# Performance work log

Measured on AMD Instinct MI355X. Metric: run time of the kernel, lower is better.

The kernel has to match this reference:

```python
import jax, jax.numpy as jnp
import numpy as np

N_NODES = 100000


def gcn_conv(x, edge_index, edge_weight, W, b):
    """PyG GCNConv: add self-loops (weight 1), symmetric deg^-1/2 norm,
    linear transform, scatter-add aggregation over destination nodes, + bias."""
    n = x.shape[0]
    src = jnp.concatenate([edge_index[0], jnp.arange(n, dtype=edge_index.dtype)])
    dst = jnp.concatenate([edge_index[1], jnp.arange(n, dtype=edge_index.dtype)])
    ew = jnp.concatenate([edge_weight, jnp.ones((n,), dtype=x.dtype)])
    # weighted degree over destinations (symmetric graph assumed as in GCN norm)
    deg = jax.ops.segment_sum(ew, dst, num_segments=n)
    dinv = jnp.where(deg > 0, jax.lax.rsqrt(deg), 0.0).astype(x.dtype)
    norm = dinv[src] * ew * dinv[dst]                    # [E+N]
    h = x @ W                                            # [N, out]
    msg = h[src] * norm[:, None]                         # gather + scale
    agg = jax.ops.segment_sum(msg, dst, num_segments=n)  # scatter-add
    return agg + b


def setup_inputs() -> dict:
    key = jax.random.key(0)
    k = jax.random.split(key, 8)
    d_in, d_hid, d_out = 128, 64, 2
    n_edges = 3200000
    x = jax.random.normal(k[0], (N_NODES, d_in), dtype=jnp.float32)
    edge_index = jax.random.randint(k[1], (2, n_edges), 0, N_NODES, dtype=jnp.int64)
    edge_weight = jax.random.uniform(k[2], (n_edges,), dtype=jnp.float32)
    # Glorot-ish init for linear weights, zeros for bias (PyG default)
    W1 = jax.random.normal(k[3], (d_in, d_hid), dtype=jnp.float32) / np.sqrt(d_in)
    b1 = jnp.zeros((d_hid,), dtype=jnp.float32)
    W2 = jax.random.normal(k[4], (d_hid, d_out), dtype=jnp.float32) / np.sqrt(d_hid)
    b2 = jnp.zeros((d_out,), dtype=jnp.float32)
    return {"x": x, "edge_index": edge_index, "edge_weight": edge_weight,
            "W1": W1, "b1": b1, "W2": W2, "b2": b2}


def reference(x, edge_index, edge_weight, W1, b1, W2, b2):
    h = gcn_conv(x, edge_index, edge_weight, W1, b1)
    h = jax.nn.relu(h)
    out = gcn_conv(h, edge_index, edge_weight, W2, b2)
    return out
```

## Files before the change

kernel.cpp:

```cpp
#include <hip/hip_runtime.h>
#include <hip/hip_bf16.h>
#include <hip/hip_fp16.h>


#define DIN  128
#define DHID 64
#define BSH  7
#define BCAP 5000
#define SCHUNK 12544
#define BMAX 800

typedef _Float16 half8 __attribute__((ext_vector_type(8)));
typedef float    f32x4 __attribute__((ext_vector_type(4)));

__global__ __launch_bounds__(1024) void k_hist(const int* __restrict__ ei,
                                               int* __restrict__ histT,
                                               int E, int chunk, int B, int C) {
    extern __shared__ int h[];
    for (int t = threadIdx.x; t < B; t += 1024) h[t] = 0;
    __syncthreads();
    int c = blockIdx.x;
    int e0 = c * chunk, e1 = min(E, e0 + chunk);
    for (int e = e0 + threadIdx.x; e < e1; e += 1024)
        atomicAdd(&h[ei[E + e] >> BSH], 1);
    __syncthreads();
    for (int t = threadIdx.x; t < B; t += 1024) histT[(size_t)t * C + c] = h[t];
}

__global__ __launch_bounds__(256) void k_scan1(int* __restrict__ histT,
                                               int* __restrict__ tot, int C) {
    __shared__ int sm[256];
    int b = blockIdx.x, t = threadIdx.x;
    size_t base = (size_t)b * C;
    int v = histT[base + t];
    sm[t] = v;
    __syncthreads();
    for (int off = 1; off < 256; off <<= 1) {
        int add = (t >= off) ? sm[t - off] : 0;
        __syncthreads();
        sm[t] += add;
        __syncthreads();
    }
    histT[base + t] = sm[t] - v;
    if (t == 255) tot[b] = sm[t];
}

__global__ __launch_bounds__(1024) void k_scan2(const int* __restrict__ tot,
                                                int* __restrict__ bb, int B) {
    __shared__ int sm[1024];
    int t = threadIdx.x;
    int v = (t < B) ? tot[t] : 0;
    sm[t] = v;
    __syncthreads();
    for (int off = 1; off < 1024; off <<= 1) {
        int add = (t >= off) ? sm[t - off] : 0;
        __syncthreads();
        sm[t] += add;
        __syncthreads();
    }
    if (t < B) {
        bb[t] = sm[t] - v;
        if (t == B - 1) bb[B] = sm[t];
    }
}

__global__ __launch_bounds__(1024) void k_scatter(const int* __restrict__ ei,
                                                  const float* __restrict__ ew,
                                                  const int* __restrict__ histT,
                                                  const int* __restrict__ bb,
                                                  int2* __restrict__ ebuf,
                                                  int E, int chunk, int B, int C) {
    __shared__ int eidx[SCHUNK];
    __shared__ int lbase[BMAX];
    __shared__ int lcur[BMAX];
    __shared__ int gbase[BMAX];
    int c = blockIdx.x, t = threadIdx.x;
    int e0 = c * chunk, e1 = min(E, e0 + chunk), m = e1 - e0;

    for (int b = t; b < B; b += 1024) lcur[b] = 0;
    __syncthreads();
    for (int q = t; q < m; q += 1024)
        atomicAdd(&lcur[ei[E + e0 + q] >> BSH], 1);
    __syncthreads();
    int v = (t < B) ? lcur[t] : 0;
    eidx[t] = v;
    __syncthreads();
    for (int off = 1; off < 1024; off <<= 1) {
        int add = (t >= off) ? eidx[t - off] : 0;
        __syncthreads();
        eidx[t] += add;
        __syncthreads();
    }
    if (t < B) {
        lbase[t] = eidx[t] - v;
        gbase[t] = histT[(size_t)t * C + c] + bb[t];
        lcur[t] = 0;
    }
    __syncthreads();
    for (int q = t; q < m; q += 1024) {
        int b = ei[E + e0 + q] >> BSH;
        int pos = lbase[b] + atomicAdd(&lcur[b], 1);
        eidx[pos] = q;
    }
    __syncthreads();
    for (int q = t; q < m; q += 1024) {
        int e = e0 + eidx[q];
        int s = ei[e];
        int d = ei[E + e];
        float w = ew[e];
        int b = d >> BSH;
        int gpos = gbase[b] + (q - lbase[b]);
        ebuf[gpos] = make_int2(s | ((d & 127) << 24), __float_as_int(w));
    }
}

__global__ __launch_bounds__(512) void k_build(const int2* __restrict__ ebuf,
                                               const int* __restrict__ bb,
                                               int* __restrict__ rp,
                                               float* __restrict__ dinv,
                                               int2* __restrict__ csw,
                                               int N, int E) {
    __shared__ int2  stage[BCAP];
    __shared__ int   cnt[128];
    __shared__ float dsum[128];
    __shared__ int   lrp[128];
    __shared__ int   cur[128];
    __shared__ int   sm[512];
    int b = blockIdx.x, t = threadIdx.x;
    if (t < 128) { cnt[t] = 0; dsum[t] = 0.0f; cur[t] = 0; }
    __syncthreads();
    int p0 = bb[b], p1 = bb[b + 1];
    int m = p1 - p0;
    bool fits = (m <= BCAP);
    for (int p = p0 + t; p < p1; p += 512) {
        int2 v = ebuf[p];
        if (fits) stage[p - p0] = v;
        int ln = (((unsigned)v.x) >> 24) & 127;
        atomicAdd(&cnt[ln], 1);
        atomicAdd(&dsum[ln], __int_as_float(v.y));
    }
    __syncthreads();
    int cv = (t < 128) ? cnt[t] : 0;
    sm[t] = cv;
    __syncthreads();
    for (int off = 1; off < 128; off <<= 1) {
        int add = (t >= off) ? sm[t - off] : 0;
        __syncthreads();
        sm[t] += add;
        __syncthreads();
    }
    if (t < 128) {
        lrp[t] = sm[t] - cv + p0;
        int d = (b << BSH) + t;
        if (d < N) {
            rp[d]   = lrp[t];
            dinv[d] = rsqrtf(1.0f + dsum[t]);
        }
    }
    if (b == 0 && t == 0) rp[N] = E;
    __syncthreads();
    for (int q = t; q < m; q += 512) {
        int2 v = fits ? stage[q] : ebuf[p0 + q];
        int ln = (((unsigned)v.x) >> 24) & 127;
        int r = atomicAdd(&cur[ln], 1);
        csw[lrp[ln] + r] = make_int2(v.x & 0xFFFFFF, v.y);
    }
}

__global__ __launch_bounds__(256) void k_gemm1(const float* __restrict__ x,
                                               const float* __restrict__ W1,
                                               __half* __restrict__ h1, int N) {
    __shared__ _Float16 As[64][136];
    __shared__ _Float16 Bs[64][136];
    int t = threadIdx.x;
    int wave = t >> 6, lane = t & 63;
    int r0 = blockIdx.x * 64;

    for (int idx = t; idx < DIN * DHID; idx += 256) {
        int k = idx >> 6, c = idx & 63;
        Bs[c][k] = (_Float16)W1[idx];
    }
    const float4* xv = (const float4*)x;
    for (int idx = t; idx < 64 * 32; idx += 256) {
        int r = idx >> 5, c4 = idx & 31;
        int rr = r0 + r;
        float4 v = (rr < N) ? xv[(size_t)rr * 32 + c4]
                            : make_float4(0.f, 0.f, 0.f, 0.f);
        As[r][c4 * 4 + 0] = (_Float16)v.x;
        As[r][c4 * 4 + 1] = (_Float16)v.y;
        As[r][c4 * 4 + 2] = (_Float16)v.z;
        As[r][c4 * 4 + 3] = (_Float16)v.w;
    }
    __syncthreads();

    int row = lane & 15;
    int kg  = lane >> 4;
    f32x4 acc0 = {0.f,0.f,0.f,0.f}, acc1 = {0.f,0.f,0.f,0.f};
    f32x4 acc2 = {0.f,0.f,0.f,0.f}, acc3 = {0.f,0.f,0.f,0.f};
#pragma unroll
    for (int kc = 0; kc < 4; ++kc) {
        half8 a = *(const half8*)&As[wave * 16 + row][kc * 32 + kg * 8];
        half8 b0 = *(const half8*)&Bs[ 0 + row][kc * 32 + kg * 8];
        half8 b1 = *(const half8*)&Bs[16 + row][kc * 32 + kg * 8];
        half8 b2 = *(const half8*)&Bs[32 + row][kc * 32 + kg * 8];
        half8 b3 = *(const half8*)&Bs[48 + row][kc * 32 + kg * 8];
        acc0 = __builtin_amdgcn_mfma_f32_16x16x32_f16(a, b0, acc0, 0, 0, 0);
        acc1 = __builtin_amdgcn_mfma_f32_16x16x32_f16(a, b1, acc1, 0, 0, 0);
        acc2 = __builtin_amdgcn_mfma_f32_16x16x32_f16(a, b2, acc2, 0, 0, 0);
        acc3 = __builtin_amdgcn_mfma_f32_16x16x32_f16(a, b3, acc3, 0, 0, 0);
    }
#pragma unroll
    for (int reg = 0; reg < 4; ++reg) {
        int rr = r0 + wave * 16 + kg * 4 + reg;
        if (rr < N) {
            int col = lane & 15;
            size_t base = (size_t)rr * DHID;
            h1[base + col +  0] = __float2half(acc0[reg]);
            h1[base + col + 16] = __float2half(acc1[reg]);
            h1[base + col + 32] = __float2half(acc2[reg]);
            h1[base + col + 48] = __float2half(acc3[reg]);
        }
    }
}

__global__ __launch_bounds__(256) void k_agg1(const __half* __restrict__ h1h,
                                              const int* __restrict__ rp,
                                              const int2* __restrict__ csw,
                                              const float* __restrict__ dinv,
                                              const float* __restrict__ b1,
                                              const float* __restrict__ W2,
                                              float* __restrict__ h2, int N) {
    int lane = threadIdx.x & 63;
    int i = (blockIdx.x * 256 + threadIdx.x) >> 6;
    if (i >= N) return;
    float bias = b1[lane];
    float w2a = W2[lane * 2];
    float w2b = W2[lane * 2 + 1];
    int s0 = __builtin_amdgcn_readfirstlane(rp[i]);
    int e0 = __builtin_amdgcn_readfirstlane(rp[i + 1]);
    float acc = 0.0f;
    int p = s0;
    for (; p + 8 <= e0; p += 8) {
        int2 eA = csw[p],     eB = csw[p + 1], eC = csw[p + 2], eD = csw[p + 3];
        int2 eE = csw[p + 4], eF = csw[p + 5], eG = csw[p + 6], eH = csw[p + 7];
        int sA = __builtin_amdgcn_readfirstlane(eA.x);
        int sB = __builtin_amdgcn_readfirstlane(eB.x);
        int sC = __builtin_amdgcn_readfirstlane(eC.x);
        int sD = __builtin_amdgcn_readfirstlane(eD.x);
        int sE = __builtin_amdgcn_readfirstlane(eE.x);
        int sF = __builtin_amdgcn_readfirstlane(eF.x);
        int sG = __builtin_amdgcn_readfirstlane(eG.x);
        int sH = __builtin_amdgcn_readfirstlane(eH.x);
        float wA = __uint_as_float(__builtin_amdgcn_readfirstlane(eA.y)) * dinv[sA];
        float wB = __uint_as_float(__builtin_amdgcn_readfirstlane(eB.y)) * dinv[sB];
        float wC = __uint_as_float(__builtin_amdgcn_readfirstlane(eC.y)) * dinv[sC];
        float wD = __uint_as_float(__builtin_amdgcn_readfirstlane(eD.y)) * dinv[sD];
        float wE = __uint_as_float(__builtin_amdgcn_readfirstlane(eE.y)) * dinv[sE];
        float wF = __uint_as_float(__builtin_amdgcn_readfirstlane(eF.y)) * dinv[sF];
        float wG = __uint_as_float(__builtin_amdgcn_readfirstlane(eG.y)) * dinv[sG];
        float wH = __uint_as_float(__builtin_amdgcn_readfirstlane(eH.y)) * dinv[sH];
        float hA = __half2float(h1h[(size_t)sA * DHID + lane]);
        float hB = __half2float(h1h[(size_t)sB * DHID + lane]);
        float hC = __half2float(h1h[(size_t)sC * DHID + lane]);
        float hD = __half2float(h1h[(size_t)sD * DHID + lane]);
        float hE = __half2float(h1h[(size_t)sE * DHID + lane]);
        float hF = __half2float(h1h[(size_t)sF * DHID + lane]);
        float hG = __half2float(h1h[(size_t)sG * DHID + lane]);
        float hH = __half2float(h1h[(size_t)sH * DHID + lane]);
        acc = fmaf(wA, hA, acc);
        acc = fmaf(wB, hB, acc);
        acc = fmaf(wC, hC, acc);
        acc = fmaf(wD, hD, acc);
        acc = fmaf(wE, hE, acc);
        acc = fmaf(wF, hF, acc);
        acc = fmaf(wG, hG, acc);
        acc = fmaf(wH, hH, acc);
    }
    for (; p + 4 <= e0; p += 4) {
        int2 eA = csw[p], eB = csw[p + 1], eC = csw[p + 2], eD = csw[p + 3];
        int sA = __builtin_amdgcn_readfirstlane(eA.x);
        int sB = __builtin_amdgcn_readfirstlane(eB.x);
        int sC = __builtin_amdgcn_readfirstlane(eC.x);
        int sD = __builtin_amdgcn_readfirstlane(eD.x);
        float wA = __uint_as_float(__builtin_amdgcn_readfirstlane(eA.y)) * dinv[sA];
        float wB = __uint_as_float(__builtin_amdgcn_readfirstlane(eB.y)) * dinv[sB];
        float wC = __uint_as_float(__builtin_amdgcn_readfirstlane(eC.y)) * dinv[sC];
        float wD = __uint_as_float(__builtin_amdgcn_readfirstlane(eD.y)) * dinv[sD];
        float hA = __half2float(h1h[(size_t)sA * DHID + lane]);
        float hB = __half2float(h1h[(size_t)sB * DHID + lane]);
        float hC = __half2float(h1h[(size_t)sC * DHID + lane]);
        float hD = __half2float(h1h[(size_t)sD * DHID + lane]);
        acc = fmaf(wA, hA, acc);
        acc = fmaf(wB, hB, acc);
        acc = fmaf(wC, hC, acc);
        acc = fmaf(wD, hD, acc);
    }
    for (; p < e0; ++p) {
        int2 eA = csw[p];
        int sA = __builtin_amdgcn_readfirstlane(eA.x);
        float wA = __uint_as_float(__builtin_amdgcn_readfirstlane(eA.y)) * dinv[sA];
        acc = fmaf(wA, __half2float(h1h[(size_t)sA * DHID + lane]), acc);
    }
    float di = dinv[i];
    acc = (acc + di * __half2float(h1h[(size_t)i * DHID + lane])) * di;
    acc = fmaxf(acc + bias, 0.0f);
    float o0 = acc * w2a, o1 = acc * w2b;
    for (int off = 32; off > 0; off >>= 1) {
        o0 += __shfl_xor(o0, off);
        o1 += __shfl_xor(o1, off);
    }
    if (lane == 0) {
        h2[i * 2]     = o0;
        h2[i * 2 + 1] = o1;
    }
}

__global__ __launch_bounds__(256) void k_prop2(const float* __restrict__ h2,
                                               const int* __restrict__ rp,
                                               const int2* __restrict__ csw,
                                               const float* __restrict__ dinv,
                                               const float* __restrict__ b2,
                                               float* __restrict__ out, int N) {
    const float2* h2v = (const float2*)h2;
    int lane = threadIdx.x & 63;
    int i = (blockIdx.x * 256 + threadIdx.x) >> 6;
    if (i >= N) return;
    int s0 = rp[i], e0 = rp[i + 1];
    float a0 = 0.0f, a1 = 0.0f;
    for (int p = s0 + lane; p < e0; p += 64) {
        int2 ed = csw[p];
        float w = __int_as_float(ed.y) * dinv[ed.x];
        float2 hv = h2v[ed.x];
        a0 = fmaf(w, hv.x, a0);
        a1 = fmaf(w, hv.y, a1);
    }
    for (int off = 32; off > 0; off >>= 1) {
        a0 += __shfl_xor(a0, off);
        a1 += __shfl_xor(a1, off);
    }
    if (lane == 0) {
        float di = dinv[i];
        out[i * 2]     = di * (a0 + di * h2[i * 2])     + b2[0];
        out[i * 2 + 1] = di * (a1 + di * h2[i * 2 + 1]) + b2[1];
    }
}

extern "C" void kernel_launch(void* const* d_in, const int* in_sizes, int n_in,
                              void* d_out, int out_size, void* d_ws, size_t ws_size,
                              hipStream_t stream) {
    const float* x  = (const float*)d_in[0];
    const int*   ei = (const int*)d_in[1];
    const float* ew = (const float*)d_in[2];
    const float* W1 = (const float*)d_in[3];
    const float* b1 = (const float*)d_in[4];
    const float* W2 = (const float*)d_in[5];
    const float* b2 = (const float*)d_in[6];
    float* out = (float*)d_out;

    const int N = in_sizes[0] / DIN;
    const int E = in_sizes[2];

    const int C = 256;
    const int B = (N + 127) >> BSH;
    const int chunk = (E + C - 1) / C;

    char* w0 = (char*)d_ws;
    float* dinv  = (float*)w0;
    int*   rp    = (int*)(dinv + N);
    int*   histT = rp + (N + 4);
    int*   tot   = histT + (size_t)B * C;
    int*   bb    = tot + B;
    size_t off_csw = ((size_t)((char*)(bb + B + 1) - w0) + 15) & ~(size_t)15;
    int2*  csw  = (int2*)(w0 + off_csw);
    int2*  ebuf = csw + E;
    __half* h1  = (__half*)ebuf;
    float* h2   = (float*)(h1 + (size_t)N * DHID);

    size_t ldsB = (size_t)B * sizeof(int);

    k_hist<<<C, 1024, ldsB, stream>>>(ei, histT, E, chunk, B, C);
    k_scan1<<<B, 256, 0, stream>>>(histT, tot, C);
    k_scan2<<<1, 1024, 0, stream>>>(tot, bb, B);
    k_scatter<<<C, 1024, 0, stream>>>(ei, ew, histT, bb, ebuf, E, chunk, B, C);
    k_build<<<B, 512, 0, stream>>>(ebuf, bb, rp, dinv, csw, N, E);

    const int GB = (N + 63) / 64;
    k_gemm1<<<GB, 256, 0, stream>>>(x, W1, h1, N);

    const int GW = ((size_t)N * 64 + 255) / 256;
    k_agg1<<<GW, 256, 0, stream>>>(h1, rp, csw, dinv, b1, W2, h2, N);
    k_prop2<<<GW, 256, 0, stream>>>(h2, rp, csw, dinv, b2, out, N);
}
```

Before: 376.8 us.

## Split hidden features into four column chunks to shrink gather working set

The GEMM now writes h1 in a chunked column-major layout of four 16-feature slabs. Aggregation runs as four passes, one per slab, each with 8 edges per wave and 8 lanes per edge, so each pass gathers from a 3.2 MB table that is more likely to stay cache-resident. The first pass writes the dinv-prescaled edge weight back into the CSR, which lets later passes and prop2 skip the dinv gather. The cost is reading the edge list four times and combining partial h2 results with atomics.

```diff
diff --git a/kernel.cpp b/kernel.cpp
--- a/kernel.cpp
+++ b/kernel.cpp
@@ -169,7 +169,7 @@
 
 __global__ __launch_bounds__(256) void k_gemm1(const float* __restrict__ x,
                                                const float* __restrict__ W1,
-                                               __half* __restrict__ h1, int N) {
+                                               __half* __restrict__ h1c, int N) {
     __shared__ _Float16 As[64][136];
     __shared__ _Float16 Bs[64][136];
     int t = threadIdx.x;
@@ -209,109 +209,87 @@
         acc2 = __builtin_amdgcn_mfma_f32_16x16x32_f16(a, b2, acc2, 0, 0, 0);
         acc3 = __builtin_amdgcn_mfma_f32_16x16x32_f16(a, b3, acc3, 0, 0, 0);
     }
+    size_t cb = (size_t)N * 16;
 #pragma unroll
     for (int reg = 0; reg < 4; ++reg) {
         int rr = r0 + wave * 16 + kg * 4 + reg;
         if (rr < N) {
             int col = lane & 15;
-            size_t base = (size_t)rr * DHID;
-            h1[base + col +  0] = __float2half(acc0[reg]);
-            h1[base + col + 16] = __float2half(acc1[reg]);
-            h1[base + col + 32] = __float2half(acc2[reg]);
-            h1[base + col + 48] = __float2half(acc3[reg]);
-        }
-    }
-}
-
-__global__ __launch_bounds__(256) void k_agg1(const __half* __restrict__ h1h,
+            size_t base = (size_t)rr * 16 + col;
+            h1c[0 * cb + base] = __float2half(acc0[reg]);
+            h1c[1 * cb + base] = __float2half(acc1[reg]);
+            h1c[2 * cb + base] = __float2half(acc2[reg]);
+            h1c[3 * cb + base] = __float2half(acc3[reg]);
+        }
+    }
+}
+
+__global__ __launch_bounds__(256) void k_aggP(const __half* __restrict__ h1c,
                                               const int* __restrict__ rp,
-                                              const int2* __restrict__ csw,
+                                              int2* __restrict__ csw,
                                               const float* __restrict__ dinv,
                                               const float* __restrict__ b1,
                                               const float* __restrict__ W2,
-                                              float* __restrict__ h2, int N) {
+                                              float* __restrict__ h2,
+                                              int N, int chunk) {
     int lane = threadIdx.x & 63;
     int i = (blockIdx.x * 256 + threadIdx.x) >> 6;
     if (i >= N) return;
-    float bias = b1[lane];
-    float w2a = W2[lane * 2];
-    float w2b = W2[lane * 2 + 1];
+    int j = lane >> 3;
+    int k = lane & 7;
+    const __half2* hb = (const __half2*)(h1c + (size_t)chunk * ((size_t)N * 16));
+    const long long* cq = (const long long*)csw;
     int s0 = __builtin_amdgcn_readfirstlane(rp[i]);
     int e0 = __builtin_amdgcn_readfirstlane(rp[i + 1]);
-    float acc = 0.0f;
-    int p = s0;
-    for (; p + 8 <= e0; p += 8) {
-        int2 eA = csw[p],     eB = csw[p + 1], eC = csw[p + 2], eD = csw[p + 3];
-        int2 eE = csw[p + 4], eF = csw[p + 5], eG = csw[p + 6], eH = csw[p + 7];
-        int sA = __builtin_amdgcn_readfirstlane(eA.x);
-        int sB = __builtin_amdgcn_readfirstlane(eB.x);
-        int sC = __builtin_amdgcn_readfirstlane(eC.x);
-        int sD = __builtin_amdgcn_readfirstlane(eD.x);
-        int sE = __builtin_amdgcn_readfirstlane(eE.x);
-        int sF = __builtin_amdgcn_readfirstlane(eF.x);
-        int sG = __builtin_amdgcn_readfirstlane(eG.x);
-        int sH = __builtin_amdgcn_readfirstlane(eH.x);
-        float wA = __uint_as_float(__builtin_amdgcn_readfirstlane(eA.y)) * dinv[sA];
-        float wB = __uint_as_float(__builtin_amdgcn_readfirstlane(eB.y)) * dinv[sB];
-        float wC = __uint_as_float(__builtin_amdgcn_readfirstlane(eC.y)) * dinv[sC];
-        float wD = __uint_as_float(__builtin_amdgcn_readfirstlane(eD.y)) * dinv[sD];
-        float wE = __uint_as_float(__builtin_amdgcn_readfirstlane(eE.y)) * dinv[sE];
-        float wF = __uint_as_float(__builtin_amdgcn_readfirstlane(eF.y)) * dinv[sF];
-        float wG = __uint_as_float(__builtin_amdgcn_readfirstlane(eG.y)) * dinv[sG];
-        float wH = __uint_as_float(__builtin_amdgcn_readfirstlane(eH.y)) * dinv[sH];
-        float hA = __half2float(h1h[(size_t)sA * DHID + lane]);
-        float hB = __half2float(h1h[(size_t)sB * DHID + lane]);
-        float hC = __half2float(h1h[(size_t)sC * DHID + lane]);
-        float hD = __half2float(h1h[(size_t)sD * DHID + lane]);
-        float hE = __half2float(h1h[(size_t)sE * DHID + lane]);
-        float hF = __half2float(h1h[(size_t)sF * DHID + lane]);
-        float hG = __half2float(h1h[(size_t)sG * DHID + lane]);
-        float hH = __half2float(h1h[(size_t)sH * DHID + lane]);
-        acc = fmaf(wA, hA, acc);
-        acc = fmaf(wB, hB, acc);
-        acc = fmaf(wC, hC, acc);
-        acc = fmaf(wD, hD, acc);
-        acc = fmaf(wE, hE, acc);
-        acc = fmaf(wF, hF, acc);
-        acc = fmaf(wG, hG, acc);
-        acc = fmaf(wH, hH, acc);
-    }
-    for (; p + 4 <= e0; p += 4) {
-        int2 eA = csw[p], eB = csw[p + 1], eC = csw[p + 2], eD = csw[p + 3];
-        int sA = __builtin_amdgcn_readfirstlane(eA.x);
-        int sB = __builtin_amdgcn_readfirstlane(eB.x);
-        int sC = __builtin_amdgcn_readfirstlane(eC.x);
-        int sD = __builtin_amdgcn_readfirstlane(eD.x);
-        float wA = __uint_as_float(__builtin_amdgcn_readfirstlane(eA.y)) * dinv[sA];
-        float wB = __uint_as_float(__builtin_amdgcn_readfirstlane(eB.y)) * dinv[sB];
-        float wC = __uint_as_float(__builtin_amdgcn_readfirstlane(eC.y)) * dinv[sC];
-        float wD = __uint_as_float(__builtin_amdgcn_readfirstlane(eD.y)) * dinv[sD];
-        float hA = __half2float(h1h[(size_t)sA * DHID + lane]);
-        float hB = __half2float(h1h[(size_t)sB * DHID + lane]);
-        float hC = __half2float(h1h[(size_t)sC * DHID + lane]);
-        float hD = __half2float(h1h[(size_t)sD * DHID + lane]);
-        acc = fmaf(wA, hA, acc);
-        acc = fmaf(wB, hB, acc);
-        acc = fmaf(wC, hC, acc);
-        acc = fmaf(wD, hD, acc);
-    }
-    for (; p < e0; ++p) {
-        int2 eA = csw[p];
-        int sA = __builtin_amdgcn_readfirstlane(eA.x);
-        float wA = __uint_as_float(__builtin_amdgcn_readfirstlane(eA.y)) * dinv[sA];
-        acc = fmaf(wA, __half2float(h1h[(size_t)sA * DHID + lane]), acc);
+    float a0 = 0.f, a1 = 0.f;
+    if (chunk == 0) {
+        for (int p = s0; p < e0; p += 8) {
+            int pe = p + j;
+            bool ok = pe < e0;
+            long long ev = ok ? __builtin_nontemporal_load(cq + pe) : 0LL;
+            int s = (int)(ev & 0xFFFFFF);
+            float wn = __int_as_float((int)(ev >> 32)) * dinv[s];
+            if (ok && k == 0) ((int*)csw)[2 * pe + 1] = __float_as_int(wn);
+            float2 hf = __half22float2(hb[(size_t)s * 8 + k]);
+            a0 = fmaf(wn, hf.x, a0);
+            a1 = fmaf(wn, hf.y, a1);
+        }
+    } else {
+        for (int p = s0; p < e0; p += 8) {
+            int pe = p + j;
+            long long ev = (pe < e0) ? __builtin_nontemporal_load(cq + pe) : 0LL;
+            int s = (int)(ev & 0xFFFFFF);
+            float wn = __int_as_float((int)(ev >> 32));
+            float2 hf = __half22float2(hb[(size_t)s * 8 + k]);
+            a0 = fmaf(wn, hf.x, a0);
+            a1 = fmaf(wn, hf.y, a1);
+        }
+    }
+    for (int off = 8; off < 64; off <<= 1) {
+        a0 += __shfl_xor(a0, off);
+        a1 += __shfl_xor(a1, off);
     }
     float di = dinv[i];
-    acc = (acc + di * __half2float(h1h[(size_t)i * DHID + lane])) * di;
-    acc = fmaxf(acc + bias, 0.0f);
-    float o0 = acc * w2a, o1 = acc * w2b;
-    for (int off = 32; off > 0; off >>= 1) {
+    float2 sf = __half22float2(hb[(size_t)i * 8 + k]);
+    a0 = fmaf(di, sf.x, a0);
+    a1 = fmaf(di, sf.y, a1);
+    int f0 = chunk * 16 + 2 * k, f1 = f0 + 1;
+    float r0 = fmaxf(fmaf(di, a0, b1[f0]), 0.0f);
+    float r1 = fmaxf(fmaf(di, a1, b1[f1]), 0.0f);
+    float o0 = r0 * W2[f0 * 2]     + r1 * W2[f1 * 2];
+    float o1 = r0 * W2[f0 * 2 + 1] + r1 * W2[f1 * 2 + 1];
+    for (int off = 1; off < 8; off <<= 1) {
         o0 += __shfl_xor(o0, off);
         o1 += __shfl_xor(o1, off);
     }
     if (lane == 0) {
-        h2[i * 2]     = o0;
-        h2[i * 2 + 1] = o1;
+        if (chunk == 0) {
+            h2[i * 2]     = o0;
+            h2[i * 2 + 1] = o1;
+        } else {
+            atomicAdd(&h2[i * 2],     o0);
+            atomicAdd(&h2[i * 2 + 1], o1);
+        }
     }
 }
 
@@ -329,7 +307,7 @@
     float a0 = 0.0f, a1 = 0.0f;
     for (int p = s0 + lane; p < e0; p += 64) {
         int2 ed = csw[p];
-        float w = __int_as_float(ed.y) * dinv[ed.x];
+        float w = __int_as_float(ed.y);
         float2 hv = h2v[ed.x];
         a0 = fmaf(w, hv.x, a0);
         a1 = fmaf(w, hv.y, a1);
@@ -373,8 +351,8 @@
     size_t off_csw = ((size_t)((char*)(bb + B + 1) - w0) + 15) & ~(size_t)15;
     int2*  csw  = (int2*)(w0 + off_csw);
     int2*  ebuf = csw + E;
-    __half* h1  = (__half*)ebuf;
-    float* h2   = (float*)(h1 + (size_t)N * DHID);
+    __half* h1c = (__half*)ebuf;
+    float* h2   = (float*)histT;
 
     size_t ldsB = (size_t)B * sizeof(int);
 
@@ -385,9 +363,10 @@
     k_build<<<B, 512, 0, stream>>>(ebuf, bb, rp, dinv, csw, N, E);
 
     const int GB = (N + 63) / 64;
-    k_gemm1<<<GB, 256, 0, stream>>>(x, W1, h1, N);
+    k_gemm1<<<GB, 256, 0, stream>>>(x, W1, h1c, N);
 
     const int GW = ((size_t)N * 64 + 255) / 256;
-    k_agg1<<<GW, 256, 0, stream>>>(h1, rp, csw, dinv, b1, W2, h2, N);
+    for (int c = 0; c < 4; ++c)
+        k_aggP<<<GW, 256, 0, stream>>>(h1c, rp, csw, dinv, b1, W2, h2, N, c);
     k_prop2<<<GW, 256, 0, stream>>>(h2, rp, csw, dinv, b2, out, N);
 }
```

After: 565.3 us. 1.5x slower.

## Precompute degree norms early and fold source dinv into stored edge weights

Applied to the files above, without the earlier changes.

The weighted in-degree is now accumulated with global float atomics in the histogram pass, and dinv is computed in a separate kernel before the scatter. The scatter then stores each edge weight already multiplied by dinv of its source, so both aggregation kernels drop a random dinv gather per edge. The aggregation inner loop is widened from 8 to 16 edges per iteration to keep more gathers in flight. The trade-off is 3.2M global atomics to 100K addresses, two extra small launches, and reuse of the histT region for h2.

```diff
diff --git a/kernel.cpp b/kernel.cpp
--- a/kernel.cpp
+++ b/kernel.cpp
@@ -13,16 +13,26 @@
 typedef _Float16 half8 __attribute__((ext_vector_type(8)));
 typedef float    f32x4 __attribute__((ext_vector_type(4)));
 
+__global__ __launch_bounds__(256) void k_zero(float* __restrict__ p, int n) {
+    int i = blockIdx.x * 256 + threadIdx.x;
+    if (i < n) p[i] = 0.0f;
+}
+
 __global__ __launch_bounds__(1024) void k_hist(const int* __restrict__ ei,
+                                               const float* __restrict__ ew,
                                                int* __restrict__ histT,
+                                               float* __restrict__ dsum,
                                                int E, int chunk, int B, int C) {
     extern __shared__ int h[];
     for (int t = threadIdx.x; t < B; t += 1024) h[t] = 0;
     __syncthreads();
     int c = blockIdx.x;
     int e0 = c * chunk, e1 = min(E, e0 + chunk);
-    for (int e = e0 + threadIdx.x; e < e1; e += 1024)
-        atomicAdd(&h[ei[E + e] >> BSH], 1);
+    for (int e = e0 + threadIdx.x; e < e1; e += 1024) {
+        int d = ei[E + e];
+        atomicAdd(&h[d >> BSH], 1);
+        atomicAdd(&dsum[d], ew[e]);
+    }
     __syncthreads();
     for (int t = threadIdx.x; t < B; t += 1024) histT[(size_t)t * C + c] = h[t];
 }
@@ -64,10 +74,17 @@
     }
 }
 
+__global__ __launch_bounds__(256) void k_dinv(const float* __restrict__ dsum,
+                                              float* __restrict__ dinv, int N) {
+    int i = blockIdx.x * 256 + threadIdx.x;
+    if (i < N) dinv[i] = rsqrtf(1.0f + dsum[i]);
+}
+
 __global__ __launch_bounds__(1024) void k_scatter(const int* __restrict__ ei,
                                                   const float* __restrict__ ew,
                                                   const int* __restrict__ histT,
                                                   const int* __restrict__ bb,
+                                                  const float* __restrict__ dinv,
                                                   int2* __restrict__ ebuf,
                                                   int E, int chunk, int B, int C) {
     __shared__ int eidx[SCHUNK];
@@ -107,27 +124,25 @@
         int e = e0 + eidx[q];
         int s = ei[e];
         int d = ei[E + e];
-        float w = ew[e];
+        float wn = ew[e] * dinv[s];
         int b = d >> BSH;
         int gpos = gbase[b] + (q - lbase[b]);
-        ebuf[gpos] = make_int2(s | ((d & 127) << 24), __float_as_int(w));
+        ebuf[gpos] = make_int2(s | ((d & 127) << 24), __float_as_int(wn));
     }
 }
 
 __global__ __launch_bounds__(512) void k_build(const int2* __restrict__ ebuf,
                                                const int* __restrict__ bb,
                                                int* __restrict__ rp,
-                                               float* __restrict__ dinv,
                                                int2* __restrict__ csw,
                                                int N, int E) {
     __shared__ int2  stage[BCAP];
     __shared__ int   cnt[128];
-    __shared__ float dsum[128];
     __shared__ int   lrp[128];
     __shared__ int   cur[128];
     __shared__ int   sm[512];
     int b = blockIdx.x, t = threadIdx.x;
-    if (t < 128) { cnt[t] = 0; dsum[t] = 0.0f; cur[t] = 0; }
+    if (t < 128) { cnt[t] = 0; cur[t] = 0; }
     __syncthreads();
     int p0 = bb[b], p1 = bb[b + 1];
     int m = p1 - p0;
@@ -137,7 +152,6 @@
         if (fits) stage[p - p0] = v;
         int ln = (((unsigned)v.x) >> 24) & 127;
         atomicAdd(&cnt[ln], 1);
-        atomicAdd(&dsum[ln], __int_as_float(v.y));
     }
     __syncthreads();
     int cv = (t < 128) ? cnt[t] : 0;
@@ -152,10 +166,7 @@
     if (t < 128) {
         lrp[t] = sm[t] - cv + p0;
         int d = (b << BSH) + t;
-        if (d < N) {
-            rp[d]   = lrp[t];
-            dinv[d] = rsqrtf(1.0f + dsum[t]);
-        }
+        if (d < N) rp[d] = lrp[t];
     }
     if (b == 0 && t == 0) rp[N] = E;
     __syncthreads();
@@ -240,66 +251,45 @@
     int e0 = __builtin_amdgcn_readfirstlane(rp[i + 1]);
     float acc = 0.0f;
     int p = s0;
-    for (; p + 8 <= e0; p += 8) {
-        int2 eA = csw[p],     eB = csw[p + 1], eC = csw[p + 2], eD = csw[p + 3];
-        int2 eE = csw[p + 4], eF = csw[p + 5], eG = csw[p + 6], eH = csw[p + 7];
-        int sA = __builtin_amdgcn_readfirstlane(eA.x);
-        int sB = __builtin_amdgcn_readfirstlane(eB.x);
-        int sC = __builtin_amdgcn_readfirstlane(eC.x);
-        int sD = __builtin_amdgcn_readfirstlane(eD.x);
-        int sE = __builtin_amdgcn_readfirstlane(eE.x);
-        int sF = __builtin_amdgcn_readfirstlane(eF.x);
-        int sG = __builtin_amdgcn_readfirstlane(eG.x);
-        int sH = __builtin_amdgcn_readfirstlane(eH.x);
-        float wA = __uint_as_float(__builtin_amdgcn_readfirstlane(eA.y)) * dinv[sA];
-        float wB = __uint_as_float(__builtin_amdgcn_readfirstlane(eB.y)) * dinv[sB];
-        float wC = __uint_as_float(__builtin_amdgcn_readfirstlane(eC.y)) * dinv[sC];
-        float wD = __uint_as_float(__builtin_amdgcn_readfirstlane(eD.y)) * dinv[sD];
-        float wE = __uint_as_float(__builtin_amdgcn_readfirstlane(eE.y)) * dinv[sE];
-        float wF = __uint_as_float(__builtin_amdgcn_readfirstlane(eF.y)) * dinv[sF];
-        float wG = __uint_as_float(__builtin_amdgcn_readfirstlane(eG.y)) * dinv[sG];
-        float wH = __uint_as_float(__builtin_amdgcn_readfirstlane(eH.y)) * dinv[sH];
-        float hA = __half2float(h1h[(size_t)sA * DHID + lane]);
-        float hB = __half2float(h1h[(size_t)sB * DHID + lane]);
-        float hC = __half2float(h1h[(size_t)sC * DHID + lane]);
-        float hD = __half2float(h1h[(size_t)sD * DHID + lane]);
-        float hE = __half2float(h1h[(size_t)sE * DHID + lane]);
-        float hF = __half2float(h1h[(size_t)sF * DHID + lane]);
-        float hG = __half2float(h1h[(size_t)sG * DHID + lane]);
-        float hH = __half2float(h1h[(size_t)sH * DHID + lane]);
-        acc = fmaf(wA, hA, acc);
-        acc = fmaf(wB, hB, acc);
-        acc = fmaf(wC, hC, acc);
-        acc = fmaf(wD, hD, acc);
-        acc = fmaf(wE, hE, acc);
-        acc = fmaf(wF, hF, acc);
-        acc = fmaf(wG, hG, acc);
-        acc = fmaf(wH, hH, acc);
+    for (; p + 16 <= e0; p += 16) {
+        int   s[16];
+        float w[16];
+#pragma unroll
+        for (int k = 0; k < 16; ++k) {
+            int2 e = csw[p + k];
+            s[k] = __builtin_amdgcn_readfirstlane(e.x);
+            w[k] = __uint_as_float(__builtin_amdgcn_readfirstlane(e.y));
+        }
+        float h[16];
+#pragma unroll
+        for (int k = 0; k < 16; ++k)
+            h[k] = __half2float(h1h[(size_t)s[k] * DHID + lane]);
+#pragma unroll
+        for (int k = 0; k < 16; ++k)
+            acc = fmaf(w[k], h[k], acc);
     }
     for (; p + 4 <= e0; p += 4) {
-        int2 eA = csw[p], eB = csw[p + 1], eC = csw[p + 2], eD = csw[p + 3];
-        int sA = __builtin_amdgcn_readfirstlane(eA.x);
-        int sB = __builtin_amdgcn_readfirstlane(eB.x);
-        int sC = __builtin_amdgcn_readfirstlane(eC.x);
-        int sD = __builtin_amdgcn_readfirstlane(eD.x);
-        float wA = __uint_as_float(__builtin_amdgcn_readfirstlane(eA.y)) * dinv[sA];
-        float wB = __uint_as_float(__builtin_amdgcn_readfirstlane(eB.y)) * dinv[sB];
-        float wC = __uint_as_float(__builtin_amdgcn_readfirstlane(eC.y)) * dinv[sC];
-        float wD = __uint_as_float(__builtin_amdgcn_readfirstlane(eD.y)) * dinv[sD];
-        float hA = __half2float(h1h[(size_t)sA * DHID + lane]);
-        float hB = __half2float(h1h[(size_t)sB * DHID + lane]);
-        float hC = __half2float(h1h[(size_t)sC * DHID + lane]);
-        float hD = __half2float(h1h[(size_t)sD * DHID + lane]);
-        acc = fmaf(wA, hA, acc);
-        acc = fmaf(wB, hB, acc);
-        acc = fmaf(wC, hC, acc);
-        acc = fmaf(wD, hD, acc);
+        int   s[4];
+        float w[4];
+#pragma unroll
+        for (int k = 0; k < 4; ++k) {
+            int2 e = csw[p + k];
+            s[k] = __builtin_amdgcn_readfirstlane(e.x);
+            w[k] = __uint_as_float(__builtin_amdgcn_readfirstlane(e.y));
+        }
+        float h[4];
+#pragma unroll
+        for (int k = 0; k < 4; ++k)
+            h[k] = __half2float(h1h[(size_t)s[k] * DHID + lane]);
+#pragma unroll
+        for (int k = 0; k < 4; ++k)
+            acc = fmaf(w[k], h[k], acc);
     }
     for (; p < e0; ++p) {
-        int2 eA = csw[p];
-        int sA = __builtin_amdgcn_readfirstlane(eA.x);
-        float wA = __uint_as_float(__builtin_amdgcn_readfirstlane(eA.y)) * dinv[sA];
-        acc = fmaf(wA, __half2float(h1h[(size_t)sA * DHID + lane]), acc);
+        int2 e = csw[p];
+        int   s = __builtin_amdgcn_readfirstlane(e.x);
+        float w = __uint_as_float(__builtin_amdgcn_readfirstlane(e.y));
+        acc = fmaf(w, __half2float(h1h[(size_t)s * DHID + lane]), acc);
     }
     float di = dinv[i];
     acc = (acc + di * __half2float(h1h[(size_t)i * DHID + lane])) * di;
@@ -329,7 +319,7 @@
     float a0 = 0.0f, a1 = 0.0f;
     for (int p = s0 + lane; p < e0; p += 64) {
         int2 ed = csw[p];
-        float w = __int_as_float(ed.y) * dinv[ed.x];
+        float w = __int_as_float(ed.y);
         float2 hv = h2v[ed.x];
         a0 = fmaf(w, hv.x, a0);
         a1 = fmaf(w, hv.y, a1);
@@ -365,7 +355,8 @@
     const int chunk = (E + C - 1) / C;
 
     char* w0 = (char*)d_ws;
-    float* dinv  = (float*)w0;
+    float* dsum  = (float*)w0;
+    float* dinv  = dsum + N;
     int*   rp    = (int*)(dinv + N);
     int*   histT = rp + (N + 4);
     int*   tot   = histT + (size_t)B * C;
@@ -374,15 +365,17 @@
     int2*  csw  = (int2*)(w0 + off_csw);
     int2*  ebuf = csw + E;
     __half* h1  = (__half*)ebuf;
-    float* h2   = (float*)(h1 + (size_t)N * DHID);
+    float* h2   = (float*)histT;
 
     size_t ldsB = (size_t)B * sizeof(int);
 
-    k_hist<<<C, 1024, ldsB, stream>>>(ei, histT, E, chunk, B, C);
+    k_zero<<<(N + 255) / 256, 256, 0, stream>>>(dsum, N);
+    k_hist<<<C, 1024, ldsB, stream>>>(ei, ew, histT, dsum, E, chunk, B, C);
     k_scan1<<<B, 256, 0, stream>>>(histT, tot, C);
     k_scan2<<<1, 1024, 0, stream>>>(tot, bb, B);
-    k_scatter<<<C, 1024, 0, stream>>>(ei, ew, histT, bb, ebuf, E, chunk, B, C);
-    k_build<<<B, 512, 0, stream>>>(ebuf, bb, rp, dinv, csw, N, E);
+    k_dinv<<<(N + 255) / 256, 256, 0, stream>>>(dsum, dinv, N);
+    k_scatter<<<C, 1024, 0, stream>>>(ei, ew, histT, bb, dinv, ebuf, E, chunk, B, C);
+    k_build<<<B, 512, 0, stream>>>(ebuf, bb, rp, csw, N, E);
 
     const int GB = (N + 63) / 64;
     k_gemm1<<<GB, 256, 0, stream>>>(x, W1, h1, N);
```

New measurement: 509.4 us. +35.2%, slower.
